# Kernel optimization log

Measured on AMD Instinct MI355X. Metric: run time of the kernel, lower is better.

## Reference

```python
import jax, jax.numpy as jnp
import numpy as np

B, T, S, H = 8, 256, 256, 512


def setup_inputs() -> dict:
    key = jax.random.key(0)
    k1, k2, k3, k4, k5, k6, k7 = jax.random.split(key, 7)
    query = jax.random.normal(k1, (B, T, H), dtype=jnp.float32)
    encoder_outputs = jax.random.normal(k2, (B, S, H), dtype=jnp.float32)
    src_lengths = jax.random.randint(k3, (B,), 1, S + 1)
    src_lengths = src_lengths.at[0].set(S)  # ensure max(lengths) == S (torch code masks to lengths.max())
    scale = 1.0 / np.sqrt(H)
    W_s = jax.random.normal(k4, (H, H), dtype=jnp.float32) * scale      # nn.Linear(H,H) weight
    W_h = jax.random.normal(k5, (H, H), dtype=jnp.float32) * scale
    v = jax.random.normal(k6, (H,), dtype=jnp.float32) * scale          # nn.Linear(H,1) weight
    W_out = jax.random.normal(k7, (H, 2 * H), dtype=jnp.float32) * scale  # nn.Linear(2H,H) weight
    return {"query": query, "encoder_outputs": encoder_outputs, "src_lengths": src_lengths,
            "W_s": W_s, "W_h": W_h, "v": v, "W_out": W_out}


def reference(query, encoder_outputs, src_lengths, W_s, W_h, v, W_out):
    # torch Linear: y = x @ W.T
    Ws_q = jnp.einsum('bth,oh->bto', query, W_s)            # (B,T,H)
    Wh_e = jnp.einsum('bsh,oh->bso', encoder_outputs, W_h)  # (B,S,H)
    # score(i,j) = v^T tanh(Ws_q_j + Wh_e_i), broadcast over (B,T,S,H)
    energies = jnp.einsum('btsh,h->bts',
                          jnp.tanh(Ws_q[:, :, None, :] + Wh_e[:, None, :, :]), v)
    mask = jnp.arange(encoder_outputs.shape[1]) < src_lengths[:, None]  # (B,S)
    energies = jnp.where(mask[:, None, :], energies, -jnp.inf)
    attn_weights = jax.nn.softmax(energies, axis=-1)        # (B,T,S)
    context = jnp.einsum('bts,bsh->bth', attn_weights, encoder_outputs)
    combined = jnp.concatenate([context, query], axis=-1)   # (B,T,2H)
    attn_out = jnp.tanh(jnp.einsum('btk,ok->bto', combined, W_out))
    return attn_out
```

## Files before the change

### kernel.cpp

```cpp
#include <hip/hip_runtime.h>
#include <hip/hip_bf16.h>


typedef __attribute__((ext_vector_type(8))) short bf16x8;
typedef __attribute__((ext_vector_type(4))) float floatx4;

#define C2LOG2E 2.8853900817779268f
#define LOG2E   1.4426950408889634f
#define NEGBIG  -1e30f

__device__ __forceinline__ float fexp2(float x) { return __builtin_amdgcn_exp2f(x); }
__device__ __forceinline__ float frcp(float x)  { return __builtin_amdgcn_rcpf(x); }
__device__ __forceinline__ float ftanh(float x) {
    return 1.0f - 2.0f * frcp(1.0f + fexp2(C2LOG2E * x));
}
__device__ __forceinline__ float fexp2x(float x) {
    return fexp2(C2LOG2E * x);
}

__device__ __forceinline__ unsigned int f2bf_bits(float f) {
    unsigned int u = __float_as_uint(f);
    return (u + 0x7fffu + ((u >> 16) & 1u)) >> 16;
}

__global__ __launch_bounds__(256) void cast_all_bf16(
    const float* __restrict__ q,  const float* __restrict__ e,
    const float* __restrict__ Ws, const float* __restrict__ Wh,
    const float* __restrict__ Wo,
    unsigned short* __restrict__ qb,  unsigned short* __restrict__ eb,
    unsigned short* __restrict__ Wsb, unsigned short* __restrict__ Whb,
    unsigned short* __restrict__ Wob)
{
    int blk = blockIdx.x;
    const float* src; unsigned short* dst; int base;
    if      (blk < 1024) { src = q;  dst = qb;  base = blk; }
    else if (blk < 2048) { src = e;  dst = eb;  base = blk - 1024; }
    else if (blk < 2304) { src = Ws; dst = Wsb; base = blk - 2048; }
    else if (blk < 2560) { src = Wh; dst = Whb; base = blk - 2304; }
    else                 { src = Wo; dst = Wob; base = blk - 2560; }
    size_t i = (size_t)base * 1024 + threadIdx.x * 4;
    float4 f = *(const float4*)(src + i);
    ushort4 o;
    o.x = (unsigned short)f2bf_bits(f.x);
    o.y = (unsigned short)f2bf_bits(f.y);
    o.z = (unsigned short)f2bf_bits(f.z);
    o.w = (unsigned short)f2bf_bits(f.w);
    *(ushort4*)(dst + i) = o;
}

__global__ __launch_bounds__(256) void gemm32x64_exp_dual(
    const unsigned short* __restrict__ Xa, const unsigned short* __restrict__ Wa,
    float* __restrict__ Ca,
    const unsigned short* __restrict__ Xb, const unsigned short* __restrict__ Wb_,
    float* __restrict__ Cb)
{
    __shared__ unsigned short sA[32 * 72];
    __shared__ unsigned short sB[64 * 72];
    const int K = 512;
    int blk = blockIdx.x;
    const unsigned short* X; const unsigned short* W; float* C;
    int mt, nt, N;
    if (blk < 512) { X = Xa; W = Wa; C = Ca; N = 512;  mt = blk >> 3; nt = blk & 7; }
    else { blk -= 512; X = Xb; W = Wb_; C = Cb; N = 2048; mt = blk >> 5; nt = blk & 31; }
    int row0 = mt * 32, col0 = nt * 64;
    int tid = threadIdx.x, lane = tid & 63, w = tid >> 6;
    int srA = tid >> 3, scA = (tid & 7) * 8;
    int srB = tid >> 2, scB = (tid & 3) * 16;
    int mw = (w & 1) * 16, nw = (w >> 1) * 32;
    int r = lane & 15, kq = (lane >> 4) * 8;

    floatx4 acc0 = {0,0,0,0}, acc1 = {0,0,0,0};
    const unsigned short* ga = X + (size_t)(row0 + srA) * K + scA;
    const unsigned short* gb = W + (size_t)(col0 + srB) * K + scB;

    for (int kb = 0; kb < 8; ++kb) {
        uint4 a0 = *(const uint4*)(ga);
        uint4 b0 = *(const uint4*)(gb);
        uint4 b1 = *(const uint4*)(gb + 8);
        ga += 64; gb += 64;
        __syncthreads();
        *(uint4*)&sA[srA * 72 + scA]     = a0;
        *(uint4*)&sB[srB * 72 + scB]     = b0;
        *(uint4*)&sB[srB * 72 + scB + 8] = b1;
        __syncthreads();
#pragma unroll
        for (int ks = 0; ks < 64; ks += 32) {
            bf16x8 af  = *(const bf16x8*)&sA[(mw + r) * 72 + ks + kq];
            bf16x8 bf0 = *(const bf16x8*)&sB[(nw + r) * 72 + ks + kq];
            bf16x8 bf1 = *(const bf16x8*)&sB[(nw + 16 + r) * 72 + ks + kq];
            acc0 = __builtin_amdgcn_mfma_f32_16x16x32_bf16(af, bf0, acc0, 0, 0, 0);
            acc1 = __builtin_amdgcn_mfma_f32_16x16x32_bf16(af, bf1, acc1, 0, 0, 0);
        }
    }
    int rq = (lane >> 4) * 4;
    float* cp = C + (size_t)(row0 + mw + rq) * N + col0 + nw + r;
#pragma unroll
    for (int i = 0; i < 4; ++i) {
        cp[(size_t)i * N]      = fexp2x(acc0[i]);
        cp[(size_t)i * N + 16] = fexp2x(acc1[i]);
    }
}

#define TQ 4
__global__ __launch_bounds__(512) void energies_v6(
    const float* __restrict__ EA,
    const float* __restrict__ EBT,
    const float* __restrict__ Vv,
    const int* __restrict__ Len,
    float* __restrict__ E)
{
    __shared__ float sA[TQ][516];
    __shared__ float sWn[512];
    __shared__ float sRed[8][TQ][130];

    int tid  = threadIdx.x;
    int lane = tid & 63;
    int w    = tid >> 6;
    int blk  = blockIdx.x;
    int b    = blk >> 7;
    int j    = (blk >> 6) & 1;
    int tq   = blk & 63;
    int len  = Len[b];
    if (j * 128 >= len) return;
    int row0g = b * 256 + tq * TQ;

    {
        int t = tid >> 7, c = (tid & 127) * 4;
        *(float4*)&sA[t][c] = *(const float4*)(EA + (size_t)(row0g + t) * 512 + c);
        sWn[tid] = -2.0f * Vv[tid];
    }
    __syncthreads();

    int h0 = w * 64;
    float acc[TQ][2] = {{0.f}};
    const float* bt = EBT + (size_t)h0 * 2048 + b * 256 + j * 128 + lane;

    float B[8], P[8];
#pragma unroll
    for (int i = 0; i < 4; ++i) {
        B[i]     = bt[(size_t)i * 2048];
        B[i + 4] = bt[(size_t)i * 2048 + 64];
    }
#pragma unroll
    for (int hh = 0; hh < 64; hh += 4) {
        if (hh + 4 < 64) {
            const float* nb = bt + (size_t)(hh + 4) * 2048;
#pragma unroll
            for (int i = 0; i < 4; ++i) {
                P[i]     = nb[(size_t)i * 2048];
                P[i + 4] = nb[(size_t)i * 2048 + 64];
            }
        }
        float4 w4 = *(const float4*)&sWn[h0 + hh];
#pragma unroll
        for (int t = 0; t < TQ; ++t) {
            float4 a4 = *(const float4*)&sA[t][h0 + hh];
#pragma unroll
            for (int u = 0; u < 2; ++u) {
                float d0 = fmaf(a4.x, B[4 * u + 0], 1.0f);
                float d1 = fmaf(a4.y, B[4 * u + 1], 1.0f);
                float d2 = fmaf(a4.z, B[4 * u + 2], 1.0f);
                float d3 = fmaf(a4.w, B[4 * u + 3], 1.0f);
                float num01 = fmaf(w4.x, d1, w4.y * d0);
                float num23 = fmaf(w4.z, d3, w4.w * d2);
                acc[t][u] = fmaf(num01, frcp(d0 * d1), acc[t][u]);
                acc[t][u] = fmaf(num23, frcp(d2 * d3), acc[t][u]);
            }
        }
#pragma unroll
        for (int i = 0; i < 8; ++i) B[i] = P[i];
    }

#pragma unroll
    for (int t = 0; t < TQ; ++t) {
        sRed[w][t][lane]      = acc[t][0];
        sRed[w][t][lane + 64] = acc[t][1];
    }
    __syncthreads();
    {
        int t = tid >> 7, s = tid & 127;
        float sum = 0.f;
#pragma unroll
        for (int ww = 0; ww < 8; ++ww) sum += sRed[ww][t][s];
        E[(size_t)(row0g + t) * 256 + j * 128 + s] = sum;
    }
}

__global__ __launch_bounds__(512) void softmax_ctx_fused(
    const float* __restrict__ E,
    const unsigned short* __restrict__ Eb,
    const int* __restrict__ Len,
    unsigned short* __restrict__ Ctx)
{
    __shared__ unsigned short EncT[64][264];
    __shared__ unsigned short sWb[64][264];
    int tid = threadIdx.x, lane = tid & 63, w = tid >> 6;
    int blk = blockIdx.x;
    int b = blk & 7, hq = (blk >> 3) & 7, tg = blk >> 6;
    int len = Len[b];

    {
        int s = tid >> 1, hg = (tid & 1) * 32;
        const ushort4* src = (const ushort4*)(Eb + (size_t)(b * 256 + s) * 512 + hq * 64 + hg);
#pragma unroll
        for (int k = 0; k < 8; ++k) {
            ushort4 u = src[k];
            EncT[hg + k * 4 + 0][s] = u.x;
            EncT[hg + k * 4 + 1][s] = u.y;
            EncT[hg + k * 4 + 2][s] = u.z;
            EncT[hg + k * 4 + 3][s] = u.w;
        }
    }
    for (int i = 0; i < 8; ++i) {
        int row = w * 8 + i;
        const float* erow = E + (size_t)(b * 256 + tg * 64 + row) * 256;
        float ev[4];
#pragma unroll
        for (int j = 0; j < 4; ++j) {
            int s = lane + 64 * j;
            ev[j] = (s < len) ? erow[s] : NEGBIG;
        }
        float m = fmaxf(fmaxf(ev[0], ev[1]), fmaxf(ev[2], ev[3]));
#pragma unroll
        for (int o = 1; o < 64; o <<= 1) m = fmaxf(m, __shfl_xor(m, o, 64));
        float wv[4], wsum = 0.f;
#pragma unroll
        for (int j = 0; j < 4; ++j) { wv[j] = fexp2((ev[j] - m) * LOG2E); wsum += wv[j]; }
#pragma unroll
        for (int o = 1; o < 64; o <<= 1) wsum += __shfl_xor(wsum, o, 64);
        float inv = frcp(wsum);
#pragma unroll
        for (int j = 0; j < 4; ++j)
            sWb[row][lane + 64 * j] = (unsigned short)f2bf_bits(wv[j] * inv);
    }
    __syncthreads();

    int mt = w & 3, npair = w >> 2;
    int t0 = mt * 16;
    int r  = lane & 15, kq = (lane >> 4) * 8;
    int n0 = npair * 32 + r;
    floatx4 acc0 = {0.f,0.f,0.f,0.f}, acc1 = {0.f,0.f,0.f,0.f};
#pragma unroll
    for (int k = 0; k < 8; ++k) {
        bf16x8 a  = *(const bf16x8*)(&sWb[t0 + r][kq + 32 * k]);
        bf16x8 b0 = *(const bf16x8*)(&EncT[n0][kq + 32 * k]);
        bf16x8 b1 = *(const bf16x8*)(&EncT[n0 + 16][kq + 32 * k]);
        acc0 = __builtin_amdgcn_mfma_f32_16x16x32_bf16(a, b0, acc0, 0, 0, 0);
        acc1 = __builtin_amdgcn_mfma_f32_16x16x32_bf16(a, b1, acc1, 0, 0, 0);
    }
    int row0 = (lane >> 4) * 4;
    unsigned short* op = Ctx + (size_t)(b * 256 + tg * 64 + t0 + row0) * 512 + hq * 64 + npair * 32 + r;
#pragma unroll
    for (int i = 0; i < 4; ++i) {
        op[i * 512]      = (unsigned short)f2bf_bits(acc0[i]);
        op[i * 512 + 16] = (unsigned short)f2bf_bits(acc1[i]);
    }
}

__global__ __launch_bounds__(256) void out_gemm32x64_tanh(
    const unsigned short* __restrict__ Ctx, const unsigned short* __restrict__ Q,
    const unsigned short* __restrict__ Wout, float* __restrict__ Out)
{
    __shared__ unsigned short sA[32 * 72];
    __shared__ unsigned short sB[64 * 72];
    const int N = 512, KW = 1024;
    int blk = blockIdx.x;
    int mt = blk >> 3, nt = blk & 7;
    int row0 = mt * 32, col0 = nt * 64;
    int tid = threadIdx.x, lane = tid & 63, w = tid >> 6;
    int srA = tid >> 3, scA = (tid & 7) * 8;
    int srB = tid >> 2, scB = (tid & 3) * 16;
    int mw = (w & 1) * 16, nw = (w >> 1) * 32;
    int r = lane & 15, kq = (lane >> 4) * 8;

    floatx4 acc0 = {0,0,0,0}, acc1 = {0,0,0,0};
    const unsigned short* gb = Wout + (size_t)(col0 + srB) * KW + scB;

    for (int kb = 0; kb < 16; ++kb) {
        const unsigned short* asrc = (kb < 8 ? Ctx : Q);
        const unsigned short* ga = asrc + (size_t)(row0 + srA) * 512 + (kb & 7) * 64 + scA;
        uint4 a0 = *(const uint4*)(ga);
        uint4 b0 = *(const uint4*)(gb);
        uint4 b1 = *(const uint4*)(gb + 8);
        gb += 64;
        __syncthreads();
        *(uint4*)&sA[srA * 72 + scA]     = a0;
        *(uint4*)&sB[srB * 72 + scB]     = b0;
        *(uint4*)&sB[srB * 72 + scB + 8] = b1;
        __syncthreads();
#pragma unroll
        for (int ks = 0; ks < 64; ks += 32) {
            bf16x8 af  = *(const bf16x8*)&sA[(mw + r) * 72 + ks + kq];
            bf16x8 bf0 = *(const bf16x8*)&sB[(nw + r) * 72 + ks + kq];
            bf16x8 bf1 = *(const bf16x8*)&sB[(nw + 16 + r) * 72 + ks + kq];
            acc0 = __builtin_amdgcn_mfma_f32_16x16x32_bf16(af, bf0, acc0, 0, 0, 0);
            acc1 = __builtin_amdgcn_mfma_f32_16x16x32_bf16(af, bf1, acc1, 0, 0, 0);
        }
    }
    int rq = (lane >> 4) * 4;
    float* op = Out + (size_t)(row0 + mw + rq) * N + col0 + nw + r;
#pragma unroll
    for (int i = 0; i < 4; ++i) {
        op[(size_t)i * N]      = ftanh(acc0[i]);
        op[(size_t)i * N + 16] = ftanh(acc1[i]);
    }
}

extern "C" void kernel_launch(void* const* d_in, const int* in_sizes, int n_in,
                              void* d_out, int out_size, void* d_ws, size_t ws_size,
                              hipStream_t stream)
{
    const float* query = (const float*)d_in[0];
    const float* enc   = (const float*)d_in[1];
    const int*   len   = (const int*)d_in[2];
    const float* Ws    = (const float*)d_in[3];
    const float* Wh    = (const float*)d_in[4];
    const float* v     = (const float*)d_in[5];
    const float* Wout  = (const float*)d_in[6];
    float* out = (float*)d_out;

    float* EA   = (float*)d_ws;
    float* EBT  = EA + 2048 * 512;
    float* E    = EBT + 512 * 2048;
    unsigned short* qb  = (unsigned short*)(E + 2048 * 256);
    unsigned short* eb  = qb + 2048 * 512;
    unsigned short* Wsb = eb + 2048 * 512;
    unsigned short* Whb = Wsb + 512 * 512;
    unsigned short* Wob = Whb + 512 * 512;
    unsigned short* ctx = Wob + 512 * 1024;

    cast_all_bf16<<<3072, 256, 0, stream>>>(query, enc, Ws, Wh, Wout,
                                            qb, eb, Wsb, Whb, Wob);
    gemm32x64_exp_dual<<<1024, 256, 0, stream>>>(qb, Wsb, EA, Whb, eb, EBT);
    energies_v6<<<1024, 512, 0, stream>>>(EA, EBT, v, len, E);
    softmax_ctx_fused<<<256, 512, 0, stream>>>(E, eb, len, ctx);
    out_gemm32x64_tanh<<<512, 256, 0, stream>>>(ctx, qb, Wob, out);
}
```

Measured before the change: 123.5 us.

## Fuse bf16 casts into GEMM loads and deepen energies prefetch

Removes the standalone cast kernel: the GEMMs and the softmax-context kernel now read fp32 inputs directly and convert to bf16 in registers before staging to shared memory. This drops one launch and a round trip through the bf16 copies, at the cost of twice the global read bytes per tile and repeated conversion, since weights are re-read by many blocks. The energies kernel also gains a second register prefetch stage (two steps ahead) to hide more latency, which raises register pressure.

```diff
diff --git a/kernel.cpp b/kernel.cpp
--- a/kernel.cpp
+++ b/kernel.cpp
@@ -22,43 +22,27 @@
     unsigned int u = __float_as_uint(f);
     return (u + 0x7fffu + ((u >> 16) & 1u)) >> 16;
 }
-
-__global__ __launch_bounds__(256) void cast_all_bf16(
-    const float* __restrict__ q,  const float* __restrict__ e,
-    const float* __restrict__ Ws, const float* __restrict__ Wh,
-    const float* __restrict__ Wo,
-    unsigned short* __restrict__ qb,  unsigned short* __restrict__ eb,
-    unsigned short* __restrict__ Wsb, unsigned short* __restrict__ Whb,
-    unsigned short* __restrict__ Wob)
-{
-    int blk = blockIdx.x;
-    const float* src; unsigned short* dst; int base;
-    if      (blk < 1024) { src = q;  dst = qb;  base = blk; }
-    else if (blk < 2048) { src = e;  dst = eb;  base = blk - 1024; }
-    else if (blk < 2304) { src = Ws; dst = Wsb; base = blk - 2048; }
-    else if (blk < 2560) { src = Wh; dst = Whb; base = blk - 2304; }
-    else                 { src = Wo; dst = Wob; base = blk - 2560; }
-    size_t i = (size_t)base * 1024 + threadIdx.x * 4;
-    float4 f = *(const float4*)(src + i);
-    ushort4 o;
-    o.x = (unsigned short)f2bf_bits(f.x);
-    o.y = (unsigned short)f2bf_bits(f.y);
-    o.z = (unsigned short)f2bf_bits(f.z);
-    o.w = (unsigned short)f2bf_bits(f.w);
-    *(ushort4*)(dst + i) = o;
+__device__ __forceinline__ unsigned int pack2bf(float a, float b) {
+    return f2bf_bits(a) | (f2bf_bits(b) << 16);
+}
+__device__ __forceinline__ uint4 pack8bf(float4 f0, float4 f1) {
+    uint4 r;
+    r.x = pack2bf(f0.x, f0.y); r.y = pack2bf(f0.z, f0.w);
+    r.z = pack2bf(f1.x, f1.y); r.w = pack2bf(f1.z, f1.w);
+    return r;
 }
 
 __global__ __launch_bounds__(256) void gemm32x64_exp_dual(
-    const unsigned short* __restrict__ Xa, const unsigned short* __restrict__ Wa,
+    const float* __restrict__ Xa, const float* __restrict__ Wa,
     float* __restrict__ Ca,
-    const unsigned short* __restrict__ Xb, const unsigned short* __restrict__ Wb_,
+    const float* __restrict__ Xb, const float* __restrict__ Wb_,
     float* __restrict__ Cb)
 {
     __shared__ unsigned short sA[32 * 72];
     __shared__ unsigned short sB[64 * 72];
     const int K = 512;
     int blk = blockIdx.x;
-    const unsigned short* X; const unsigned short* W; float* C;
+    const float* X; const float* W; float* C;
     int mt, nt, N;
     if (blk < 512) { X = Xa; W = Wa; C = Ca; N = 512;  mt = blk >> 3; nt = blk & 7; }
     else { blk -= 512; X = Xb; W = Wb_; C = Cb; N = 2048; mt = blk >> 5; nt = blk & 31; }
@@ -70,14 +54,17 @@
     int r = lane & 15, kq = (lane >> 4) * 8;
 
     floatx4 acc0 = {0,0,0,0}, acc1 = {0,0,0,0};
-    const unsigned short* ga = X + (size_t)(row0 + srA) * K + scA;
-    const unsigned short* gb = W + (size_t)(col0 + srB) * K + scB;
+    const float* ga = X + (size_t)(row0 + srA) * K + scA;
+    const float* gb = W + (size_t)(col0 + srB) * K + scB;
 
     for (int kb = 0; kb < 8; ++kb) {
-        uint4 a0 = *(const uint4*)(ga);
-        uint4 b0 = *(const uint4*)(gb);
-        uint4 b1 = *(const uint4*)(gb + 8);
+        float4 fa0 = ((const float4*)ga)[0], fa1 = ((const float4*)ga)[1];
+        float4 fb0 = ((const float4*)gb)[0], fb1 = ((const float4*)gb)[1];
+        float4 fb2 = ((const float4*)gb)[2], fb3 = ((const float4*)gb)[3];
         ga += 64; gb += 64;
+        uint4 a0 = pack8bf(fa0, fa1);
+        uint4 b0 = pack8bf(fb0, fb1);
+        uint4 b1 = pack8bf(fb2, fb3);
         __syncthreads();
         *(uint4*)&sA[srA * 72 + scA]     = a0;
         *(uint4*)&sB[srB * 72 + scB]     = b0;
@@ -102,7 +89,7 @@
 }
 
 #define TQ 4
-__global__ __launch_bounds__(512) void energies_v6(
+__global__ __launch_bounds__(512) void energies_v7(
     const float* __restrict__ EA,
     const float* __restrict__ EBT,
     const float* __restrict__ Vv,
@@ -135,20 +122,28 @@
     float acc[TQ][2] = {{0.f}};
     const float* bt = EBT + (size_t)h0 * 2048 + b * 256 + j * 128 + lane;
 
-    float B[8], P[8];
+    float B[8], P[8], PP[8];
 #pragma unroll
     for (int i = 0; i < 4; ++i) {
         B[i]     = bt[(size_t)i * 2048];
         B[i + 4] = bt[(size_t)i * 2048 + 64];
     }
+    {
+        const float* nb = bt + (size_t)4 * 2048;
+#pragma unroll
+        for (int i = 0; i < 4; ++i) {
+            P[i]     = nb[(size_t)i * 2048];
+            P[i + 4] = nb[(size_t)i * 2048 + 64];
+        }
+    }
 #pragma unroll
     for (int hh = 0; hh < 64; hh += 4) {
-        if (hh + 4 < 64) {
-            const float* nb = bt + (size_t)(hh + 4) * 2048;
+        if (hh + 8 < 64) {
+            const float* nb = bt + (size_t)(hh + 8) * 2048;
 #pragma unroll
             for (int i = 0; i < 4; ++i) {
-                P[i]     = nb[(size_t)i * 2048];
-                P[i + 4] = nb[(size_t)i * 2048 + 64];
+                PP[i]     = nb[(size_t)i * 2048];
+                PP[i + 4] = nb[(size_t)i * 2048 + 64];
             }
         }
         float4 w4 = *(const float4*)&sWn[h0 + hh];
@@ -168,7 +163,7 @@
             }
         }
 #pragma unroll
-        for (int i = 0; i < 8; ++i) B[i] = P[i];
+        for (int i = 0; i < 8; ++i) { B[i] = P[i]; P[i] = PP[i]; }
     }
 
 #pragma unroll
@@ -188,7 +183,7 @@
 
 __global__ __launch_bounds__(512) void softmax_ctx_fused(
     const float* __restrict__ E,
-    const unsigned short* __restrict__ Eb,
+    const float* __restrict__ Enc,
     const int* __restrict__ Len,
     unsigned short* __restrict__ Ctx)
 {
@@ -201,14 +196,14 @@
 
     {
         int s = tid >> 1, hg = (tid & 1) * 32;
-        const ushort4* src = (const ushort4*)(Eb + (size_t)(b * 256 + s) * 512 + hq * 64 + hg);
+        const float4* src = (const float4*)(Enc + (size_t)(b * 256 + s) * 512 + hq * 64 + hg);
 #pragma unroll
         for (int k = 0; k < 8; ++k) {
-            ushort4 u = src[k];
-            EncT[hg + k * 4 + 0][s] = u.x;
-            EncT[hg + k * 4 + 1][s] = u.y;
-            EncT[hg + k * 4 + 2][s] = u.z;
-            EncT[hg + k * 4 + 3][s] = u.w;
+            float4 f = src[k];
+            EncT[hg + k * 4 + 0][s] = (unsigned short)f2bf_bits(f.x);
+            EncT[hg + k * 4 + 1][s] = (unsigned short)f2bf_bits(f.y);
+            EncT[hg + k * 4 + 2][s] = (unsigned short)f2bf_bits(f.z);
+            EncT[hg + k * 4 + 3][s] = (unsigned short)f2bf_bits(f.w);
         }
     }
     for (int i = 0; i < 8; ++i) {
@@ -258,8 +253,8 @@
 }
 
 __global__ __launch_bounds__(256) void out_gemm32x64_tanh(
-    const unsigned short* __restrict__ Ctx, const unsigned short* __restrict__ Q,
-    const unsigned short* __restrict__ Wout, float* __restrict__ Out)
+    const unsigned short* __restrict__ Ctx, const float* __restrict__ Qf,
+    const float* __restrict__ Woutf, float* __restrict__ Out)
 {
     __shared__ unsigned short sA[32 * 72];
     __shared__ unsigned short sB[64 * 72];
@@ -274,15 +269,21 @@
     int r = lane & 15, kq = (lane >> 4) * 8;
 
     floatx4 acc0 = {0,0,0,0}, acc1 = {0,0,0,0};
-    const unsigned short* gb = Wout + (size_t)(col0 + srB) * KW + scB;
+    const float* gb = Woutf + (size_t)(col0 + srB) * KW + scB;
 
     for (int kb = 0; kb < 16; ++kb) {
-        const unsigned short* asrc = (kb < 8 ? Ctx : Q);
-        const unsigned short* ga = asrc + (size_t)(row0 + srA) * 512 + (kb & 7) * 64 + scA;
-        uint4 a0 = *(const uint4*)(ga);
-        uint4 b0 = *(const uint4*)(gb);
-        uint4 b1 = *(const uint4*)(gb + 8);
+        uint4 a0;
+        if (kb < 8) {
+            a0 = *(const uint4*)(Ctx + (size_t)(row0 + srA) * 512 + kb * 64 + scA);
+        } else {
+            const float* gq = Qf + (size_t)(row0 + srA) * 512 + (kb - 8) * 64 + scA;
+            a0 = pack8bf(((const float4*)gq)[0], ((const float4*)gq)[1]);
+        }
+        float4 fb0 = ((const float4*)gb)[0], fb1 = ((const float4*)gb)[1];
+        float4 fb2 = ((const float4*)gb)[2], fb3 = ((const float4*)gb)[3];
         gb += 64;
+        uint4 b0 = pack8bf(fb0, fb1);
+        uint4 b1 = pack8bf(fb2, fb3);
         __syncthreads();
         *(uint4*)&sA[srA * 72 + scA]     = a0;
         *(uint4*)&sB[srB * 72 + scB]     = b0;
@@ -322,17 +323,10 @@
     float* EA   = (float*)d_ws;
     float* EBT  = EA + 2048 * 512;
     float* E    = EBT + 512 * 2048;
-    unsigned short* qb  = (unsigned short*)(E + 2048 * 256);
-    unsigned short* eb  = qb + 2048 * 512;
-    unsigned short* Wsb = eb + 2048 * 512;
-    unsigned short* Whb = Wsb + 512 * 512;
-    unsigned short* Wob = Whb + 512 * 512;
-    unsigned short* ctx = Wob + 512 * 1024;
-
-    cast_all_bf16<<<3072, 256, 0, stream>>>(query, enc, Ws, Wh, Wout,
-                                            qb, eb, Wsb, Whb, Wob);
-    gemm32x64_exp_dual<<<1024, 256, 0, stream>>>(qb, Wsb, EA, Whb, eb, EBT);
-    energies_v6<<<1024, 512, 0, stream>>>(EA, EBT, v, len, E);
-    softmax_ctx_fused<<<256, 512, 0, stream>>>(E, eb, len, ctx);
-    out_gemm32x64_tanh<<<512, 256, 0, stream>>>(ctx, qb, Wob, out);
-}
+    unsigned short* ctx = (unsigned short*)(E + 2048 * 256);
+
+    gemm32x64_exp_dual<<<1024, 256, 0, stream>>>(query, Ws, EA, Wh, enc, EBT);
+    energies_v7<<<1024, 512, 0, stream>>>(EA, EBT, v, len, E);
+    softmax_ctx_fused<<<256, 512, 0, stream>>>(E, enc, len, ctx);
+    out_gemm32x64_tanh<<<512, 256, 0, stream>>>(ctx, query, Wout, out);
+}
```

Measured after the change: 134.6 us. +9.0%, slower.
